# Kernel tuning notes

Hardware: AMD Instinct MI355X
Metric: run time of the kernel (lower is better)

## Reference

```python
import jax, jax.numpy as jnp
import numpy as np

N_NODES = 50000
N_EDGES = 1600000
D_FEAT = 128
ORDER = 2


def setup_inputs() -> dict:
    key = jax.random.key(0)
    k1, k2, k3, k4 = jax.random.split(key, 4)
    x = jax.random.normal(k1, (N_NODES, D_FEAT), dtype=jnp.float32)
    adj_row = jax.random.randint(k2, (N_EDGES,), 0, N_NODES, dtype=jnp.int32)
    adj_col = jax.random.randint(k3, (N_EDGES,), 0, N_NODES, dtype=jnp.int32)
    adj_vals = jax.random.uniform(k4, (N_EDGES,), dtype=jnp.float32)
    return {"x": x, "adj_row": adj_row, "adj_col": adj_col, "adj_vals": adj_vals}


def reference(x, adj_row, adj_col, adj_vals):
    # SGC propagation: x <- A @ x, repeated `order` times.
    # A is sparse COO: A[row, col] = vals; spmm(A, x)[i] = sum_e vals[e]*x[col[e]] into row[e].
    for _ in range(ORDER):
        msgs = adj_vals[:, None] * x[adj_col]          # [E, F] gathered messages
        x = jax.ops.segment_sum(msgs, adj_row, num_segments=N_NODES)  # [N, F]
    return x
```

## Files before the change

### kernel.cpp

```cpp
#include <hip/hip_runtime.h>
#include <hip/hip_fp16.h>

#define N_NODES 50000
#define N_EDGES 1600000
#define D_FEAT  128
#define NB      196
#define BCAP    8704
#define SPAIR_STRIDE (BCAP * 2)
#define S_OUT_CAP 9216
#define OVF_CAP  8192

#define P1_WGS   400
#define P1_ROUND 4096
#define P1_CAP   38

__device__ __forceinline__ unsigned short f2bf(float f) {
    union { float f; unsigned u; } v; v.f = f;
    unsigned r = v.u + 0x7fff + ((v.u >> 16) & 1);
    return (unsigned short)(r >> 16);
}
__device__ __forceinline__ float bf_lo(unsigned w) {
    union { unsigned u; float f; } v; v.u = w << 16; return v.f;
}
__device__ __forceinline__ float bf_hi(unsigned w) {
    union { unsigned u; float f; } v; v.u = w & 0xffff0000u; return v.f;
}

__global__ __launch_bounds__(256) void conv_kernel(
    const float2* __restrict__ xin, unsigned* __restrict__ xb,
    int* __restrict__ gcnt)
{
    if (blockIdx.x == 0 && threadIdx.x <= NB)
        gcnt[threadIdx.x] = 0;
    int t = blockIdx.x * blockDim.x + threadIdx.x;
    if (t < N_NODES * (D_FEAT / 2)) {
        float2 f = xin[t];
        xb[t] = ((unsigned)f2bf(f.y) << 16) | (unsigned)f2bf(f.x);
    }
}

__global__ __launch_bounds__(256) void p1_bin_kernel(
    const int* __restrict__ row, const int* __restrict__ col,
    const float* __restrict__ val,
    int* __restrict__ gcnt, uint2* __restrict__ sedge, uint2* __restrict__ ovf)
{
    __shared__ uint2    s_buf[NB * P1_CAP];
    __shared__ unsigned s_cnt[NB];
    __shared__ int      s_base[NB];

    int wg = blockIdx.x, t = threadIdx.x;
    int e0 = (int)((long)wg * N_EDGES / P1_WGS);
    int e1 = (int)((long)(wg + 1) * N_EDGES / P1_WGS);

    for (int rbase = e0; rbase < e1; rbase += P1_ROUND) {
        int rend = rbase + P1_ROUND; if (rend > e1) rend = e1;
        for (int i = t; i < NB; i += 256) s_cnt[i] = 0;
        __syncthreads();
        for (int e = rbase + t; e < rend; e += 256) {
            int r = row[e];
            int b = r >> 8;
            uint2 rec;
            rec.x = ((unsigned)r << 16) | (unsigned)col[e];
            rec.y = __float_as_uint(val[e]);
            unsigned pos = atomicAdd(&s_cnt[b], 1u);
            if (pos < P1_CAP) {
                s_buf[b * P1_CAP + pos] = rec;
            } else {
                int p = atomicAdd(&gcnt[b], 1);
                if (p < BCAP) sedge[(long)b * BCAP + p] = rec;
                else {
                    int q = atomicAdd(&gcnt[NB], 1);
                    if (q < OVF_CAP) ovf[q] = rec;
                }
            }
        }
        __syncthreads();
        if (t < NB) {
            int c = (int)s_cnt[t]; if (c > P1_CAP) c = P1_CAP;
            s_base[t] = (c > 0) ? atomicAdd(&gcnt[t], c) : 0;
        }
        __syncthreads();
        if (t < NB) {
            int c = (int)s_cnt[t]; if (c > P1_CAP) c = P1_CAP;
            int gb = s_base[t];
            for (int i = 0; i < c; ++i) {
                int p = gb + i;
                if (p < BCAP) sedge[(long)t * BCAP + p] = s_buf[t * P1_CAP + i];
                else {
                    int q = atomicAdd(&gcnt[NB], 1);
                    if (q < OVF_CAP) ovf[q] = s_buf[t * P1_CAP + i];
                }
            }
        }
        __syncthreads();
    }
}

__global__ __launch_bounds__(256) void p2_sort_kernel(
    const int* __restrict__ gcnt, const uint2* __restrict__ sedge,
    const uint2* __restrict__ ovf,
    unsigned* __restrict__ spair, int2* __restrict__ row_se)
{
    __shared__ unsigned s_out[S_OUT_CAP];
    __shared__ int s_cnt[256];
    __shared__ int s_cur[256];

    int b = blockIdx.x, t = threadIdx.x;
    int cnt = gcnt[b]; if (cnt > BCAP) cnt = BCAP;
    int ovn = gcnt[NB]; if (ovn > OVF_CAP) ovn = OVF_CAP;
    int row0 = b << 8;
    long sbase = (long)b * BCAP;

    s_cnt[t] = 0;
    __syncthreads();
    for (int i = t; i < cnt; i += 256) {
        int fr = (int)(sedge[sbase + i].x >> 16) - row0;
        atomicAdd(&s_cnt[fr], 1);
    }
    for (int i = t; i < ovn; i += 256) {
        int r = (int)(ovf[i].x >> 16);
        if ((r >> 8) == b) atomicAdd(&s_cnt[r - row0], 1);
    }
    __syncthreads();
    int orig = s_cnt[t];
    __syncthreads();
    for (int off = 1; off < 256; off <<= 1) {
        int u = (t >= off) ? s_cnt[t - off] : 0;
        __syncthreads();
        s_cnt[t] += u;
        __syncthreads();
    }
    int excl  = s_cnt[t] - orig;
    int total = s_cnt[255];
    int r = row0 + t;
    if (r < N_NODES) row_se[r] = make_int2(b * SPAIR_STRIDE + excl, orig);
    s_cur[t] = excl;
    __syncthreads();

    if (total <= S_OUT_CAP) {
        for (int i = t; i < cnt; i += 256) {
            uint2 rec = sedge[sbase + i];
            int fr = (int)(rec.x >> 16) - row0;
            int p = atomicAdd(&s_cur[fr], 1);
            unsigned short hv = __half_as_ushort(__float2half(__uint_as_float(rec.y)));
            s_out[p] = ((rec.x & 0xffffu) << 16) | (unsigned)hv;
        }
        for (int i = t; i < ovn; i += 256) {
            uint2 rec = ovf[i];
            int rr = (int)(rec.x >> 16);
            if ((rr >> 8) == b) {
                int p = atomicAdd(&s_cur[rr - row0], 1);
                unsigned short hv = __half_as_ushort(__float2half(__uint_as_float(rec.y)));
                s_out[p] = ((rec.x & 0xffffu) << 16) | (unsigned)hv;
            }
        }
        __syncthreads();
        for (int i = t; i < total; i += 256)
            spair[(long)b * SPAIR_STRIDE + i] = s_out[i];
    } else {
        for (int i = t; i < cnt; i += 256) {
            uint2 rec = sedge[sbase + i];
            int fr = (int)(rec.x >> 16) - row0;
            int p = atomicAdd(&s_cur[fr], 1);
            unsigned short hv = __half_as_ushort(__float2half(__uint_as_float(rec.y)));
            spair[(long)b * SPAIR_STRIDE + p] = ((rec.x & 0xffffu) << 16) | (unsigned)hv;
        }
    }
}

template <bool WRITE_BF16>
__global__ __launch_bounds__(256) void spmm_csr_bf2_kernel(
    const int2*     __restrict__ row_se,
    const unsigned* __restrict__ spair,
    const unsigned* __restrict__ xb,
    unsigned* __restrict__ outb,
    float*    __restrict__ outf)
{
    int wave = (blockIdx.x * blockDim.x + threadIdx.x) >> 6;
    int lane = threadIdx.x & 63;
    int half  = lane >> 5;
    int fl    = lane & 31;
    int hbase = lane & 32;
    int row   = wave * 2 + half;
    if (row >= N_NODES) return;

    const int4 s4 = ((const int4*)row_se)[wave];
    int mystart = half ? s4.z : s4.x;
    int myn     = half ? s4.w : s4.y;
    int nmax    = (s4.y > s4.w) ? s4.y : s4.w;

    float acc0 = 0.f, acc1 = 0.f, acc2 = 0.f, acc3 = 0.f;

    for (int base = 0; base < nmax; base += 32) {
        int idx = base + fl;
        unsigned rec = (idx < myn) ? spair[mystart + idx] : 0u;
        int   c = (int)(rec >> 16);
        float v = __half2float(__ushort_as_half((unsigned short)(rec & 0xffffu)));

        int steps = nmax - base; if (steps > 32) steps = 32;
        int j = 0;
        for (; j + 8 <= steps; j += 8) {
            int   cc[8];
            float vv[8];
            uint2 ww[8];
            #pragma unroll
            for (int k = 0; k < 8; ++k) {
                cc[k] = __shfl(c, hbase + j + k, 64);
                vv[k] = __shfl(v, hbase + j + k, 64);
            }
            #pragma unroll
            for (int k = 0; k < 8; ++k)
                ww[k] = *(const uint2*)(xb + (long)cc[k] * (D_FEAT / 2) + fl * 2);
            #pragma unroll
            for (int k = 0; k < 8; ++k) {
                acc0 += vv[k] * bf_lo(ww[k].x);
                acc1 += vv[k] * bf_hi(ww[k].x);
                acc2 += vv[k] * bf_lo(ww[k].y);
                acc3 += vv[k] * bf_hi(ww[k].y);
            }
        }
        for (; j < steps; ++j) {
            int   cj = __shfl(c, hbase + j, 64);
            float vj = __shfl(v, hbase + j, 64);
            uint2 w = *(const uint2*)(xb + (long)cj * (D_FEAT / 2) + fl * 2);
            acc0 += vj * bf_lo(w.x);
            acc1 += vj * bf_hi(w.x);
            acc2 += vj * bf_lo(w.y);
            acc3 += vj * bf_hi(w.y);
        }
    }

    if (WRITE_BF16) {
        uint2 w;
        w.x = ((unsigned)f2bf(acc1) << 16) | (unsigned)f2bf(acc0);
        w.y = ((unsigned)f2bf(acc3) << 16) | (unsigned)f2bf(acc2);
        *(uint2*)(outb + (long)row * (D_FEAT / 2) + fl * 2) = w;
    } else {
        *(float4*)(outf + (long)row * D_FEAT + fl * 4) =
            make_float4(acc0, acc1, acc2, acc3);
    }
}

__global__ __launch_bounds__(256) void spmm_atomic_kernel(
    const int* __restrict__ row, const int* __restrict__ col,
    const float* __restrict__ vals, const float* __restrict__ xin,
    float* __restrict__ xout)
{
    long tid   = (long)blockIdx.x * blockDim.x + threadIdx.x;
    int  edge  = (int)(tid >> 5);
    int  chunk = (int)(tid & 31);
    if (edge >= N_EDGES) return;
    int   r = row[edge];
    int   c = col[edge];
    float v = vals[edge];
    const float4 xv = ((const float4*)(xin + (long)c * D_FEAT))[chunk];
    float* dst = xout + (long)r * D_FEAT + chunk * 4;
    unsafeAtomicAdd(dst + 0, v * xv.x);
    unsafeAtomicAdd(dst + 1, v * xv.y);
    unsafeAtomicAdd(dst + 2, v * xv.z);
    unsafeAtomicAdd(dst + 3, v * xv.w);
}

static inline size_t align_up(size_t x, size_t a) { return (x + a - 1) & ~(a - 1); }

extern "C" void kernel_launch(void* const* d_in, const int* in_sizes, int n_in,
                              void* d_out, int out_size, void* d_ws, size_t ws_size,
                              hipStream_t stream) {
    const float* x        = (const float*)d_in[0];
    const int*   adj_row  = (const int*)d_in[1];
    const int*   adj_col  = (const int*)d_in[2];
    const float* adj_vals = (const float*)d_in[3];
    float*       out      = (float*)d_out;

    const size_t bf_bytes = (size_t)N_NODES * (D_FEAT / 2) * sizeof(unsigned);

    char*     ws      = (char*)d_ws;
    size_t    off     = 0;
    unsigned* xb      = (unsigned*)(ws + off); off = align_up(off + bf_bytes, 512);
    unsigned* tmpb    = (unsigned*)(ws + off); off = align_up(off + bf_bytes, 512);
    uint2*    sedge   = (uint2*)   (ws + off); off = align_up(off + (size_t)NB * BCAP * 8, 512);
    int2*     row_se  = (int2*)    (ws + off); off = align_up(off + (size_t)(NB * 256) * 8, 512);
    int*      gcnt    = (int*)     (ws + off); off = align_up(off + (NB + 1) * sizeof(int), 512);
    uint2*    ovf     = (uint2*)   (ws + off); off = align_up(off + (size_t)OVF_CAP * 8, 512);
    const size_t needed = off;

    unsigned* spair = (unsigned*)sedge;

    const int block = 256;

    if (ws_size >= needed) {
        int cgrid = (N_NODES * (D_FEAT / 2) + block - 1) / block;
        conv_kernel<<<cgrid, block, 0, stream>>>((const float2*)x, xb, gcnt);
        p1_bin_kernel<<<P1_WGS, block, 0, stream>>>(adj_row, adj_col, adj_vals,
                                                    gcnt, sedge, ovf);
        p2_sort_kernel<<<NB, block, 0, stream>>>(gcnt, sedge, ovf, spair, row_se);

        int nwaves = (N_NODES + 1) / 2;
        int ngrid  = (int)(((long)nwaves * 64 + block - 1) / block);
        spmm_csr_bf2_kernel<true><<<ngrid, block, 0, stream>>>(
            row_se, spair, xb, tmpb, (float*)nullptr);
        spmm_csr_bf2_kernel<false><<<ngrid, block, 0, stream>>>(
            row_se, spair, tmpb, (unsigned*)nullptr, out);
    } else {
        float* tmp = (float*)ws;
        const size_t feat_bytes = (size_t)N_NODES * D_FEAT * sizeof(float);
        hipMemsetAsync(tmp, 0, feat_bytes, stream);
        hipMemsetAsync(out, 0, feat_bytes, stream);
        long total_threads = (long)N_EDGES * 32;
        long grid = (total_threads + block - 1) / block;
        spmm_atomic_kernel<<<dim3((unsigned)grid), dim3(block), 0, stream>>>(
            adj_row, adj_col, adj_vals, x, tmp);
        spmm_atomic_kernel<<<dim3((unsigned)grid), dim3(block), 0, stream>>>(
            adj_row, adj_col, adj_vals, tmp, out);
    }
}
```

Before: 226.1 us.

## Use nontemporal loads/stores across pipeline and widen sort kernel to 1024 threads

Replaces streaming global loads and stores in the conversion, binning, sort and SpMM kernels with nontemporal builtins so single-use data is kept from polluting cache. The sort kernel now launches 1024 threads per block, with the per-row scan guarded to the first 256 threads, to raise parallelism on the bucket passes. The SpMM early exit moves to a per-wave check. Nontemporal hints on data that is read again, such as spair, which the second SpMM pass reuses, may reduce cache hits.

```diff
diff --git a/kernel.cpp b/kernel.cpp
--- a/kernel.cpp
+++ b/kernel.cpp
@@ -9,10 +9,16 @@
 #define SPAIR_STRIDE (BCAP * 2)
 #define S_OUT_CAP 9216
 #define OVF_CAP  8192
+#define NWAVES  (N_NODES / 2)
 
 #define P1_WGS   400
 #define P1_ROUND 4096
 #define P1_CAP   38
+
+typedef unsigned u32x2 __attribute__((ext_vector_type(2)));
+typedef int      i32x4 __attribute__((ext_vector_type(4)));
+typedef float    f32x2 __attribute__((ext_vector_type(2)));
+typedef float    f32x4 __attribute__((ext_vector_type(4)));
 
 __device__ __forceinline__ unsigned short f2bf(float f) {
     union { float f; unsigned u; } v; v.f = f;
@@ -34,7 +40,7 @@
         gcnt[threadIdx.x] = 0;
     int t = blockIdx.x * blockDim.x + threadIdx.x;
     if (t < N_NODES * (D_FEAT / 2)) {
-        float2 f = xin[t];
+        f32x2 f = __builtin_nontemporal_load((const f32x2*)xin + t);
         xb[t] = ((unsigned)f2bf(f.y) << 16) | (unsigned)f2bf(f.x);
     }
 }
@@ -57,18 +63,22 @@
         for (int i = t; i < NB; i += 256) s_cnt[i] = 0;
         __syncthreads();
         for (int e = rbase + t; e < rend; e += 256) {
-            int r = row[e];
+            int   r = __builtin_nontemporal_load(row + e);
+            int   c = __builtin_nontemporal_load(col + e);
+            float v = __builtin_nontemporal_load(val + e);
             int b = r >> 8;
             uint2 rec;
-            rec.x = ((unsigned)r << 16) | (unsigned)col[e];
-            rec.y = __float_as_uint(val[e]);
+            rec.x = ((unsigned)r << 16) | (unsigned)c;
+            rec.y = __float_as_uint(v);
             unsigned pos = atomicAdd(&s_cnt[b], 1u);
             if (pos < P1_CAP) {
                 s_buf[b * P1_CAP + pos] = rec;
             } else {
                 int p = atomicAdd(&gcnt[b], 1);
-                if (p < BCAP) sedge[(long)b * BCAP + p] = rec;
-                else {
+                if (p < BCAP) {
+                    u32x2 rv = {rec.x, rec.y};
+                    __builtin_nontemporal_store(rv, (u32x2*)(sedge + (long)b * BCAP + p));
+                } else {
                     int q = atomicAdd(&gcnt[NB], 1);
                     if (q < OVF_CAP) ovf[q] = rec;
                 }
@@ -85,8 +95,11 @@
             int gb = s_base[t];
             for (int i = 0; i < c; ++i) {
                 int p = gb + i;
-                if (p < BCAP) sedge[(long)t * BCAP + p] = s_buf[t * P1_CAP + i];
-                else {
+                if (p < BCAP) {
+                    uint2 rec = s_buf[t * P1_CAP + i];
+                    u32x2 rv = {rec.x, rec.y};
+                    __builtin_nontemporal_store(rv, (u32x2*)(sedge + (long)t * BCAP + p));
+                } else {
                     int q = atomicAdd(&gcnt[NB], 1);
                     if (q < OVF_CAP) ovf[q] = s_buf[t * P1_CAP + i];
                 }
@@ -96,7 +109,7 @@
     }
 }
 
-__global__ __launch_bounds__(256) void p2_sort_kernel(
+__global__ __launch_bounds__(1024) void p2_sort_kernel(
     const int* __restrict__ gcnt, const uint2* __restrict__ sedge,
     const uint2* __restrict__ ovf,
     unsigned* __restrict__ spair, int2* __restrict__ row_se)
@@ -111,41 +124,44 @@
     int row0 = b << 8;
     long sbase = (long)b * BCAP;
 
-    s_cnt[t] = 0;
+    if (t < 256) s_cnt[t] = 0;
     __syncthreads();
-    for (int i = t; i < cnt; i += 256) {
-        int fr = (int)(sedge[sbase + i].x >> 16) - row0;
+    for (int i = t; i < cnt; i += 1024) {
+        u32x2 rv = __builtin_nontemporal_load((const u32x2*)(sedge + sbase + i));
+        int fr = (int)(rv.x >> 16) - row0;
         atomicAdd(&s_cnt[fr], 1);
     }
-    for (int i = t; i < ovn; i += 256) {
+    for (int i = t; i < ovn; i += 1024) {
         int r = (int)(ovf[i].x >> 16);
         if ((r >> 8) == b) atomicAdd(&s_cnt[r - row0], 1);
     }
     __syncthreads();
-    int orig = s_cnt[t];
+    int orig = (t < 256) ? s_cnt[t] : 0;
     __syncthreads();
     for (int off = 1; off < 256; off <<= 1) {
-        int u = (t >= off) ? s_cnt[t - off] : 0;
-        __syncthreads();
-        s_cnt[t] += u;
-        __syncthreads();
-    }
-    int excl  = s_cnt[t] - orig;
+        int u = (t >= off && t < 256) ? s_cnt[t - off] : 0;
+        __syncthreads();
+        if (t < 256) s_cnt[t] += u;
+        __syncthreads();
+    }
     int total = s_cnt[255];
-    int r = row0 + t;
-    if (r < N_NODES) row_se[r] = make_int2(b * SPAIR_STRIDE + excl, orig);
-    s_cur[t] = excl;
+    if (t < 256) {
+        int excl = s_cnt[t] - orig;
+        int r = row0 + t;
+        if (r < N_NODES) row_se[r] = make_int2(b * SPAIR_STRIDE + excl, orig);
+        s_cur[t] = excl;
+    }
     __syncthreads();
 
     if (total <= S_OUT_CAP) {
-        for (int i = t; i < cnt; i += 256) {
-            uint2 rec = sedge[sbase + i];
-            int fr = (int)(rec.x >> 16) - row0;
+        for (int i = t; i < cnt; i += 1024) {
+            u32x2 rv = __builtin_nontemporal_load((const u32x2*)(sedge + sbase + i));
+            int fr = (int)(rv.x >> 16) - row0;
             int p = atomicAdd(&s_cur[fr], 1);
-            unsigned short hv = __half_as_ushort(__float2half(__uint_as_float(rec.y)));
-            s_out[p] = ((rec.x & 0xffffu) << 16) | (unsigned)hv;
-        }
-        for (int i = t; i < ovn; i += 256) {
+            unsigned short hv = __half_as_ushort(__float2half(__uint_as_float(rv.y)));
+            s_out[p] = ((rv.x & 0xffffu) << 16) | (unsigned)hv;
+        }
+        for (int i = t; i < ovn; i += 1024) {
             uint2 rec = ovf[i];
             int rr = (int)(rec.x >> 16);
             if ((rr >> 8) == b) {
@@ -155,10 +171,10 @@
             }
         }
         __syncthreads();
-        for (int i = t; i < total; i += 256)
-            spair[(long)b * SPAIR_STRIDE + i] = s_out[i];
+        for (int i = t; i < total; i += 1024)
+            __builtin_nontemporal_store(s_out[i], spair + (long)b * SPAIR_STRIDE + i);
     } else {
-        for (int i = t; i < cnt; i += 256) {
+        for (int i = t; i < cnt; i += 1024) {
             uint2 rec = sedge[sbase + i];
             int fr = (int)(rec.x >> 16) - row0;
             int p = atomicAdd(&s_cur[fr], 1);
@@ -177,14 +193,14 @@
     float*    __restrict__ outf)
 {
     int wave = (blockIdx.x * blockDim.x + threadIdx.x) >> 6;
+    if (wave >= NWAVES) return;
     int lane = threadIdx.x & 63;
     int half  = lane >> 5;
     int fl    = lane & 31;
     int hbase = lane & 32;
     int row   = wave * 2 + half;
-    if (row >= N_NODES) return;
-
-    const int4 s4 = ((const int4*)row_se)[wave];
+
+    const i32x4 s4 = __builtin_nontemporal_load((const i32x4*)row_se + wave);
     int mystart = half ? s4.z : s4.x;
     int myn     = half ? s4.w : s4.y;
     int nmax    = (s4.y > s4.w) ? s4.y : s4.w;
@@ -193,7 +209,8 @@
 
     for (int base = 0; base < nmax; base += 32) {
         int idx = base + fl;
-        unsigned rec = (idx < myn) ? spair[mystart + idx] : 0u;
+        unsigned rec = 0;
+        if (idx < myn) rec = __builtin_nontemporal_load(spair + mystart + idx);
         int   c = (int)(rec >> 16);
         float v = __half2float(__ushort_as_half((unsigned short)(rec & 0xffffu)));
 
@@ -231,13 +248,13 @@
     }
 
     if (WRITE_BF16) {
-        uint2 w;
+        u32x2 w;
         w.x = ((unsigned)f2bf(acc1) << 16) | (unsigned)f2bf(acc0);
         w.y = ((unsigned)f2bf(acc3) << 16) | (unsigned)f2bf(acc2);
-        *(uint2*)(outb + (long)row * (D_FEAT / 2) + fl * 2) = w;
+        __builtin_nontemporal_store(w, (u32x2*)(outb + (long)row * (D_FEAT / 2) + fl * 2));
     } else {
-        *(float4*)(outf + (long)row * D_FEAT + fl * 4) =
-            make_float4(acc0, acc1, acc2, acc3);
+        f32x4 w = {acc0, acc1, acc2, acc3};
+        __builtin_nontemporal_store(w, (f32x4*)(outf + (long)row * D_FEAT + fl * 4));
     }
 }
 
@@ -293,10 +310,9 @@
         conv_kernel<<<cgrid, block, 0, stream>>>((const float2*)x, xb, gcnt);
         p1_bin_kernel<<<P1_WGS, block, 0, stream>>>(adj_row, adj_col, adj_vals,
                                                     gcnt, sedge, ovf);
-        p2_sort_kernel<<<NB, block, 0, stream>>>(gcnt, sedge, ovf, spair, row_se);
-
-        int nwaves = (N_NODES + 1) / 2;
-        int ngrid  = (int)(((long)nwaves * 64 + block - 1) / block);
+        p2_sort_kernel<<<NB, 1024, 0, stream>>>(gcnt, sedge, ovf, spair, row_se);
+
+        int ngrid = (int)(((long)NWAVES * 64 + block - 1) / block);
         spmm_csr_bf2_kernel<true><<<ngrid, block, 0, stream>>>(
             row_se, spair, xb, tmpb, (float*)nullptr);
         spmm_csr_bf2_kernel<false><<<ngrid, block, 0, stream>>>(
```

Result: slower. 259.7 us (+14.9%).
